# Performance work log

Hardware: AMD Instinct MI355X
Metric: run time of the kernel (lower is better)

Reference implementation:

```python
import jax, jax.numpy as jnp
import numpy as np

NUM_FILTER = 256
CAPS_LEN = 8
NUM_EMOTIONS = 8
OUT_DIM = 16
NUM_CHANNEL = 25
TIME_LEN = 25
NUM_CAPS = NUM_CHANNEL * TIME_LEN * (NUM_FILTER // CAPS_LEN)  # 20000
NUM_ITERATIONS = 3


def setup_inputs() -> dict:
    key = jax.random.key(0)
    ks = jax.random.split(key, 10)
    B = 32
    x = jax.random.normal(ks[0], (B, 54, 54), jnp.float32)
    conv1_w = jax.random.normal(ks[1], (NUM_FILTER, 1, 6, 6), jnp.float32) * 0.05
    conv1_b = jax.random.normal(ks[2], (NUM_FILTER,), jnp.float32) * 0.01
    conv2_w = jax.random.normal(ks[3], (NUM_FILTER, NUM_FILTER, 6, 6), jnp.float32) * 0.01
    conv2_b = jax.random.normal(ks[4], (NUM_FILTER,), jnp.float32) * 0.01
    conv3_w = jax.random.normal(ks[5], (NUM_FILTER, 2 * NUM_FILTER, 1, 1), jnp.float32) * 0.05
    conv3_b = jax.random.normal(ks[6], (NUM_FILTER,), jnp.float32) * 0.01
    # PrimaryCaps: one Linear(caps_len -> caps_len) per capsule, batched as [nc, out, in]
    pc_w = jax.random.normal(ks[7], (NUM_CAPS, CAPS_LEN, CAPS_LEN), jnp.float32) * 0.1
    pc_b = jax.random.normal(ks[8], (NUM_CAPS, CAPS_LEN), jnp.float32) * 0.1
    # EmotionCaps transform W: [nc, num_emotions, out_dim, in_dim]
    W = jax.random.normal(ks[9], (NUM_CAPS, NUM_EMOTIONS, OUT_DIM, CAPS_LEN), jnp.float32) * 0.05
    return {"x": x, "conv1_w": conv1_w, "conv1_b": conv1_b, "conv2_w": conv2_w,
            "conv2_b": conv2_b, "conv3_w": conv3_w, "conv3_b": conv3_b,
            "pc_w": pc_w, "pc_b": pc_b, "W": W}


def _conv(x, w, b, stride):
    y = jax.lax.conv_general_dilated(x, w, (stride, stride), 'VALID',
                                     dimension_numbers=('NCHW', 'OIHW', 'NCHW'))
    return y + b[None, :, None, None]


def _squash(s):
    # scale = |s|^2 / (1 + |s|^2); out = scale * s / (|s| + 1e-8)
    n2 = jnp.sum(s * s, axis=-1, keepdims=True)
    n = jnp.sqrt(n2)
    return (n2 / (1.0 + n2)) * s / (n + 1e-8)


def reference(x, conv1_w, conv1_b, conv2_w, conv2_b, conv3_w, conv3_b, pc_w, pc_b, W):
    x4 = x[:, None]                                    # [B,1,54,54]
    x1 = jax.nn.relu(_conv(x4, conv1_w, conv1_b, 2))   # [B,F,25,25]
    y = jnp.pad(x1, ((0, 0), (0, 0), (2, 3), (2, 3)))  # ZeroPad2d((2,3,2,3))
    y = jax.nn.relu(_conv(y, conv2_w, conv2_b, 1))     # [B,F,25,25]
    z = jax.nn.relu(jnp.concatenate([x1, y], axis=1))  # [B,2F,25,25]
    z = _conv(z, conv3_w, conv3_b, 1)                  # [B,F,25,25]
    B, F, H, Wd = z.shape
    # flatten to capsules: [B, F//caps_len, caps_len, H*W] -> [B, nc, caps_len]
    caps = z.reshape(B, F // CAPS_LEN, CAPS_LEN, H * Wd)
    caps = caps.transpose(0, 1, 3, 2).reshape(B, NUM_CAPS, CAPS_LEN)
    # PrimaryCaps: per-capsule linear, batched as a single einsum
    u = jnp.einsum('bni,noi->bno', caps, pc_w) + pc_b[None]   # [B,nc,caps_len]
    # EmotionCaps: u_hat[b,n,e,o] = W[n,e,o,i] u[b,n,i]
    u_hat = jnp.einsum('bni,neoi->bneo', u, W)                # [B,nc,ne,out_dim]
    b = jnp.zeros((B, NUM_CAPS, NUM_EMOTIONS), u.dtype)
    v = None
    for r in range(NUM_ITERATIONS):
        c = jax.nn.softmax(b, axis=2)[..., None]              # [B,nc,ne,1]
        v = _squash(jnp.sum(c * u_hat, axis=1))               # [B,ne,out_dim]
        if r < NUM_ITERATIONS - 1:
            b = b + jnp.einsum('bneo,beo->bne', u_hat, v)
    return jnp.linalg.norm(v, axis=-1)                        # [B,ne]
```

## Files before the change

kernel.cpp:

```cpp
#include <hip/hip_runtime.h>

typedef unsigned short u16;
typedef __attribute__((ext_vector_type(8))) short bf16x8;
typedef __attribute__((ext_vector_type(4))) float floatx4;

#define NPIX 625
#define NCAPS 20000
#define K2 9216

__device__ __forceinline__ u16 f2bf(float f) {
  unsigned u = __float_as_uint(f);
  return (u16)((u + 0x7fffu + ((u >> 16) & 1u)) >> 16);
}

#define GLDS16(g, l) __builtin_amdgcn_global_load_lds( \
    (const __attribute__((address_space(1))) void*)(g), \
    (__attribute__((address_space(3))) void*)(l), 16, 0, 0)

__global__ void prep_weights(const float* __restrict__ w2, const float* __restrict__ w3,
                             u16* __restrict__ A2, u16* __restrict__ A3) {
  int idx = blockIdx.x * 256 + threadIdx.x;
  if (idx < 256 * 36 * 256) {
    int oc = idx / 9216, r = idx % 9216;
    int t = r >> 8, c = r & 255;
    A2[idx] = f2bf(w2[(oc * 256 + c) * 36 + t]);
  } else {
    int j = idx - 256 * 36 * 256;
    if (j < 256 * 512) A3[j] = f2bf(w3[j]);
  }
}

__global__ void prep_wbs(const float* __restrict__ W, u16* __restrict__ Wbs) {
  int r = blockIdx.x * 256 + threadIdx.x;
  int n = r >> 7, eo = r & 127;
  int e = eo >> 4, o = eo & 15;
  const float* src = W + n * 1024 + eo * 8;
  const float4 v0 = *(const float4*)src;
  const float4 v1 = *(const float4*)(src + 4);
  u16* dst = Wbs + n * 1088 + e * 136 + o * 8;
  ushort4 p0, p1;
  p0.x = f2bf(v0.x); p0.y = f2bf(v0.y); p0.z = f2bf(v0.z); p0.w = f2bf(v0.w);
  p1.x = f2bf(v1.x); p1.y = f2bf(v1.y); p1.z = f2bf(v1.z); p1.w = f2bf(v1.w);
  *(ushort4*)dst = p0;
  *(ushort4*)(dst + 4) = p1;
}

__global__ void conv1_kernel(const float* __restrict__ x, const float* __restrict__ w1,
                             const float* __restrict__ b1, u16* __restrict__ x1p) {
  int blk = blockIdx.x;
  int b = blk / 25, i = blk % 25;
  int f = threadIdx.x;
  float wreg[36];
#pragma unroll
  for (int k = 0; k < 36; k++) wreg[k] = w1[f * 36 + k];
  float bias = b1[f];
  const float* xb = x + b * 54 * 54 + (2 * i) * 54;
  for (int j = 0; j < 25; j++) {
    float acc = bias;
#pragma unroll
    for (int ki = 0; ki < 6; ki++)
#pragma unroll
      for (int kj = 0; kj < 6; kj++)
        acc = fmaf(xb[ki * 54 + 2 * j + kj], wreg[ki * 6 + kj], acc);
    x1p[(((b * 30 + i + 2) * 30) + (j + 2)) * 256 + f] = f2bf(fmaxf(acc, 0.f));
  }
}

__global__ __launch_bounds__(256) void conv2_gemm(const u16* __restrict__ A2,
    const u16* __restrict__ x1p, float* __restrict__ P) {
  __shared__ u16 As0[128 * 32];
  __shared__ u16 Bs0[128 * 32];
  __shared__ u16 As1[128 * 32];
  __shared__ u16 Bs1[128 * 32];
  const int tid = threadIdx.x;
  const int lane = tid & 63, wave = tid >> 6;
  const int mtile = blockIdx.x, ntile = blockIdx.y, kt = blockIdx.z;

  const int seg0 = tid, seg1 = tid + 256;
  const u16* gA0 = A2 + (mtile * 128 + (seg0 >> 2)) * K2 + (seg0 & 3) * 8 + kt * 4608;
  const u16* gA1 = A2 + (mtile * 128 + (seg1 >> 2)) * K2 + (seg1 & 3) * 8 + kt * 4608;

  auto pixbase = [&](int seg) {
    int n = ntile * 128 + (seg >> 2);
    if (n > NCAPS - 1) n = NCAPS - 1;
    int b = n / NPIX, p = n % NPIX;
    int i = p / 25, j = p % 25;
    return ((b * 30 + i) * 30 + j) * 256 + (seg & 3) * 8;
  };
  const u16* gb0 = x1p + pixbase(seg0);
  const u16* gb1 = x1p + pixbase(seg1);

  floatx4 acc[4][4] = {};
  const int wm = wave & 1, wn = wave >> 1;
  const int lrow = lane & 15, kgrp = lane >> 4;

  int kj = 0;
  int boff = 3 * kt * 30 * 256;
  for (int t = 0; t < 18; t++) {
#pragma unroll 1
    for (int cc = 0; cc < 8; cc += 2) {
      const int b0 = boff + cc * 32;
      GLDS16(gA0, As0 + seg0 * 8);
      GLDS16(gA1, As0 + seg1 * 8);
      GLDS16(gA0 + 32, As1 + seg0 * 8);
      GLDS16(gA1 + 32, As1 + seg1 * 8);
      GLDS16(gb0 + b0, Bs0 + seg0 * 8);
      GLDS16(gb1 + b0, Bs0 + seg1 * 8);
      GLDS16(gb0 + b0 + 32, Bs1 + seg0 * 8);
      GLDS16(gb1 + b0 + 32, Bs1 + seg1 * 8);
      gA0 += 64; gA1 += 64;
      __syncthreads();
      bf16x8 af[4], bfr[4];
#pragma unroll
      for (int tt = 0; tt < 4; tt++) {
        af[tt]  = *(const bf16x8*)(As0 + (wm * 64 + tt * 16 + lrow) * 32 + kgrp * 8);
        bfr[tt] = *(const bf16x8*)(Bs0 + (wn * 64 + tt * 16 + lrow) * 32 + kgrp * 8);
      }
#pragma unroll
      for (int tm = 0; tm < 4; tm++)
#pragma unroll
        for (int tn = 0; tn < 4; tn++)
          acc[tm][tn] = __builtin_amdgcn_mfma_f32_16x16x32_bf16(af[tm], bfr[tn], acc[tm][tn], 0, 0, 0);
#pragma unroll
      for (int tt = 0; tt < 4; tt++) {
        af[tt]  = *(const bf16x8*)(As1 + (wm * 64 + tt * 16 + lrow) * 32 + kgrp * 8);
        bfr[tt] = *(const bf16x8*)(Bs1 + (wn * 64 + tt * 16 + lrow) * 32 + kgrp * 8);
      }
#pragma unroll
      for (int tm = 0; tm < 4; tm++)
#pragma unroll
        for (int tn = 0; tn < 4; tn++)
          acc[tm][tn] = __builtin_amdgcn_mfma_f32_16x16x32_bf16(af[tm], bfr[tn], acc[tm][tn], 0, 0, 0);
      __syncthreads();
    }
    boff += 256;
    kj++;
    if (kj == 6) { kj = 0; boff += 6144; }
  }

  float* Pk = P + kt * 5120000;
  const int nb = ntile * 128 + wn * 64;
  const int ocb = mtile * 128 + wm * 64 + kgrp * 4;
#pragma unroll
  for (int tn = 0; tn < 4; tn++) {
    int n = nb + tn * 16 + lrow;
    if (n < NCAPS) {
#pragma unroll
      for (int tm = 0; tm < 4; tm++) {
        int oc = ocb + tm * 16;
        float4 v;
        v.x = acc[tm][tn][0]; v.y = acc[tm][tn][1];
        v.z = acc[tm][tn][2]; v.w = acc[tm][tn][3];
        *(float4*)(Pk + n * 256 + oc) = v;
      }
    }
  }
}

__global__ void conv2_red(const float* __restrict__ P, const float* __restrict__ bias2,
                          u16* __restrict__ y) {
  const int idx = blockIdx.x * 256 + threadIdx.x;
  const float4 a = *(const float4*)(P + idx * 4);
  const float4 b = *(const float4*)(P + 5120000 + idx * 4);
  const float4 bs = *(const float4*)(bias2 + ((idx * 4) & 255));
  ushort4 pk;
  pk.x = f2bf(fmaxf(a.x + b.x + bs.x, 0.f));
  pk.y = f2bf(fmaxf(a.y + b.y + bs.y, 0.f));
  pk.z = f2bf(fmaxf(a.z + b.z + bs.z, 0.f));
  pk.w = f2bf(fmaxf(a.w + b.w + bs.w, 0.f));
  *(ushort4*)(y + idx * 4) = pk;
}

__global__ __launch_bounds__(256) void conv3_gemm(const u16* __restrict__ A3,
    const u16* __restrict__ x1p, const u16* __restrict__ y,
    const float* __restrict__ bias3, float* __restrict__ z) {
  __shared__ u16 As[128 * 32];
  __shared__ u16 Bs[128 * 32];
  const int tid = threadIdx.x;
  const int lane = tid & 63, wave = tid >> 6;
  const int mtile = blockIdx.x, ntile = blockIdx.y;

  const int seg0 = tid, seg1 = tid + 256;
  const u16* ga0 = A3 + (mtile * 128 + (seg0 >> 2)) * 512 + (seg0 & 3) * 8;
  const u16* ga1 = A3 + (mtile * 128 + (seg1 >> 2)) * 512 + (seg1 & 3) * 8;

  auto mkbases = [&](int seg, const u16*& gx, const u16*& gy) {
    int n = ntile * 128 + (seg >> 2);
    if (n > NCAPS - 1) n = NCAPS - 1;
    int b = n / NPIX, p = n % NPIX;
    int i = p / 25, j = p % 25;
    gx = x1p + ((b * 30 + i + 2) * 30 + (j + 2)) * 256 + (seg & 3) * 8;
    gy = y + n * 256 + (seg & 3) * 8;
  };
  const u16 *gx0, *gy0, *gx1, *gy1;
  mkbases(seg0, gx0, gy0);
  mkbases(seg1, gx1, gy1);

  floatx4 acc[4][4] = {};
  const int wm = wave & 1, wn = wave >> 1;
  const int lrow = lane & 15, kgrp = lane >> 4;

  for (int kc = 0; kc < 16; kc++) {
    const u16* s0 = (kc < 8) ? (gx0 + kc * 32) : (gy0 + (kc - 8) * 32);
    const u16* s1 = (kc < 8) ? (gx1 + kc * 32) : (gy1 + (kc - 8) * 32);
    GLDS16(ga0 + kc * 32, As + seg0 * 8);
    GLDS16(ga1 + kc * 32, As + seg1 * 8);
    GLDS16(s0, Bs + seg0 * 8);
    GLDS16(s1, Bs + seg1 * 8);
    __syncthreads();
    bf16x8 af[4], bfr[4];
#pragma unroll
    for (int tt = 0; tt < 4; tt++) {
      af[tt]  = *(const bf16x8*)(As + (wm * 64 + tt * 16 + lrow) * 32 + kgrp * 8);
      bfr[tt] = *(const bf16x8*)(Bs + (wn * 64 + tt * 16 + lrow) * 32 + kgrp * 8);
    }
#pragma unroll
    for (int tm = 0; tm < 4; tm++)
#pragma unroll
      for (int tn = 0; tn < 4; tn++)
        acc[tm][tn] = __builtin_amdgcn_mfma_f32_16x16x32_bf16(af[tm], bfr[tn], acc[tm][tn], 0, 0, 0);
    __syncthreads();
  }

  const int nb = ntile * 128 + wn * 64;
  const int fb = mtile * 128 + wm * 64 + kgrp * 4;
#pragma unroll
  for (int tn = 0; tn < 4; tn++) {
    int n = nb + tn * 16 + lrow;
    if (n < NCAPS) {
#pragma unroll
      for (int tm = 0; tm < 4; tm++) {
        int f0 = fb + tm * 16;
        float4 v;
        v.x = acc[tm][tn][0] + bias3[f0 + 0];
        v.y = acc[tm][tn][1] + bias3[f0 + 1];
        v.z = acc[tm][tn][2] + bias3[f0 + 2];
        v.w = acc[tm][tn][3] + bias3[f0 + 3];
        *(float4*)(z + n * 256 + f0) = v;
      }
    }
  }
}


__device__ __forceinline__ float dot8v(float4 a0, float4 a1, float4 b0, float4 b1) {
  float s = a0.x * b0.x;
  s = fmaf(a0.y, b0.y, s); s = fmaf(a0.z, b0.z, s); s = fmaf(a0.w, b0.w, s);
  s = fmaf(a1.x, b1.x, s); s = fmaf(a1.y, b1.y, s);
  s = fmaf(a1.z, b1.z, s); s = fmaf(a1.w, b1.w, s);
  return s;
}

__device__ __forceinline__ float dotrow(uint4 w, float4 ua, float4 ub) {
  float s = __uint_as_float(w.x << 16) * ua.x;
  s = fmaf(__uint_as_float(w.x & 0xffff0000u), ua.y, s);
  s = fmaf(__uint_as_float(w.y << 16), ua.z, s);
  s = fmaf(__uint_as_float(w.y & 0xffff0000u), ua.w, s);
  s = fmaf(__uint_as_float(w.z << 16), ub.x, s);
  s = fmaf(__uint_as_float(w.z & 0xffff0000u), ub.y, s);
  s = fmaf(__uint_as_float(w.w << 16), ub.z, s);
  s = fmaf(__uint_as_float(w.w & 0xffff0000u), ub.w, s);
  return s;
}

__global__ void caps_u(const float* __restrict__ z, const float* __restrict__ pcw,
                       const float* __restrict__ pcb, float* __restrict__ u) {
  const int tid = threadIdx.x;
  const int b = tid >> 3, o = tid & 7;
  for (int k = 0; k < 8; k++) {
    const int n = blockIdx.x * 8 + k;
    const int g = n / NPIX, p = n % NPIX;
    const float* zp = z + (b * NPIX + p) * 256 + g * 8;
    float4 c0 = *(const float4*)zp;
    float4 c1 = *(const float4*)(zp + 4);
    const float* pw = pcw + n * 64 + o * 8;
    float4 w0 = *(const float4*)pw;
    float4 w1 = *(const float4*)(pw + 4);
    u[n * 256 + tid] = pcb[n * 8 + o] + dot8v(w0, w1, c0, c1);
  }
}

__global__ void caps_u2(const float* __restrict__ z, const float* __restrict__ pcw,
                        const float* __restrict__ pcb, unsigned* __restrict__ u2) {
  const int tid = threadIdx.x;
  const int b = tid >> 3, o = tid & 7;
  for (int k = 0; k < 8; k++) {
    const int n = blockIdx.x * 8 + k;
    const int g = n / NPIX, p = n % NPIX;
    const float* zp = z + (b * NPIX + p) * 256 + g * 8;
    float4 c0 = *(const float4*)zp;
    float4 c1 = *(const float4*)(zp + 4);
    const float* pw = pcw + n * 64 + o * 8;
    float4 w0 = *(const float4*)pw;
    float4 w1 = *(const float4*)(pw + 4);
    const float myu = pcb[n * 8 + o] + dot8v(w0, w1, c0, c1);
    const float partner = __shfl_xor(myu, 1, 64);
    if (!(o & 1)) {
      unsigned pk = (unsigned)f2bf(myu) | ((unsigned)f2bf(partner) << 16);
      u2[n * 128 + b * 4 + (o >> 1)] = pk;
    }
  }
}

__global__ __launch_bounds__(256, 4) void caps_accb2(const unsigned* __restrict__ u2,
    const u16* __restrict__ Wbs, const float* __restrict__ vsum,
    float* __restrict__ Spart) {
  __shared__ u16 Ws[16 * 1088];
  const int tid = threadIdx.x;
  const int b = tid >> 3, e = tid & 7;
  const int n0 = blockIdx.x * 16;

  const u16* gsrc = Wbs + n0 * 1088;
#pragma unroll
  for (int k = 0; k < 9; k++) {
    const int idx = k * 256 + tid;
    if (idx < 2176) GLDS16(gsrc + idx * 8, Ws + idx * 8);
  }

  const float* vp = vsum + tid * 16;
  const float4 V0 = *(const float4*)vp;
  const float4 V1 = *(const float4*)(vp + 4);
  const float4 V2 = *(const float4*)(vp + 8);
  const float4 V3 = *(const float4*)(vp + 12);
  float s0 = 0.f, s1 = 0.f, s2 = 0.f, s3 = 0.f, s4 = 0.f, s5 = 0.f, s6 = 0.f, s7 = 0.f;
  float s8 = 0.f, s9 = 0.f, s10 = 0.f, s11 = 0.f, s12 = 0.f, s13 = 0.f, s14 = 0.f, s15 = 0.f;

  __syncthreads();

  for (int it = 0; it < 16; it++) {
    const int n = n0 + it;
    const uint4 up = *(const uint4*)(u2 + n * 128 + b * 4);
    float4 ua, ub;
    ua.x = __uint_as_float(up.x << 16); ua.y = __uint_as_float(up.x & 0xffff0000u);
    ua.z = __uint_as_float(up.y << 16); ua.w = __uint_as_float(up.y & 0xffff0000u);
    ub.x = __uint_as_float(up.z << 16); ub.y = __uint_as_float(up.z & 0xffff0000u);
    ub.z = __uint_as_float(up.w << 16); ub.w = __uint_as_float(up.w & 0xffff0000u);

    const u16* Wn = Ws + it * 1088 + e * 136;
    float h0, h1, h2, h3, h4, h5, h6, h7, h8, h9, h10, h11, h12, h13, h14, h15;
#define ROW(o, H) { uint4 w = *(const uint4*)(Wn + (o) * 8); H = dotrow(w, ua, ub); }
    ROW(0, h0)   ROW(1, h1)   ROW(2, h2)   ROW(3, h3)
    ROW(4, h4)   ROW(5, h5)   ROW(6, h6)   ROW(7, h7)
    ROW(8, h8)   ROW(9, h9)   ROW(10, h10) ROW(11, h11)
    ROW(12, h12) ROW(13, h13) ROW(14, h14) ROW(15, h15)
#undef ROW
    float blog = h0 * V0.x;
    blog = fmaf(h1, V0.y, blog);  blog = fmaf(h2, V0.z, blog);  blog = fmaf(h3, V0.w, blog);
    blog = fmaf(h4, V1.x, blog);  blog = fmaf(h5, V1.y, blog);  blog = fmaf(h6, V1.z, blog);
    blog = fmaf(h7, V1.w, blog);  blog = fmaf(h8, V2.x, blog);  blog = fmaf(h9, V2.y, blog);
    blog = fmaf(h10, V2.z, blog); blog = fmaf(h11, V2.w, blog); blog = fmaf(h12, V3.x, blog);
    blog = fmaf(h13, V3.y, blog); blog = fmaf(h14, V3.z, blog); blog = fmaf(h15, V3.w, blog);
    float m = blog;
    m = fmaxf(m, __shfl_xor(m, 1, 64));
    m = fmaxf(m, __shfl_xor(m, 2, 64));
    m = fmaxf(m, __shfl_xor(m, 4, 64));
    float ex = __expf(blog - m);
    float ss = ex;
    ss += __shfl_xor(ss, 1, 64);
    ss += __shfl_xor(ss, 2, 64);
    ss += __shfl_xor(ss, 4, 64);
    const float c = ex / ss;
    s0 = fmaf(c, h0, s0);   s1 = fmaf(c, h1, s1);   s2 = fmaf(c, h2, s2);   s3 = fmaf(c, h3, s3);
    s4 = fmaf(c, h4, s4);   s5 = fmaf(c, h5, s5);   s6 = fmaf(c, h6, s6);   s7 = fmaf(c, h7, s7);
    s8 = fmaf(c, h8, s8);   s9 = fmaf(c, h9, s9);   s10 = fmaf(c, h10, s10); s11 = fmaf(c, h11, s11);
    s12 = fmaf(c, h12, s12); s13 = fmaf(c, h13, s13); s14 = fmaf(c, h14, s14); s15 = fmaf(c, h15, s15);
  }
  float* Sp = Spart + blockIdx.x * 4096 + tid * 16;
  *(float4*)(Sp + 0)  = make_float4(s0, s1, s2, s3);
  *(float4*)(Sp + 4)  = make_float4(s4, s5, s6, s7);
  *(float4*)(Sp + 8)  = make_float4(s8, s9, s10, s11);
  *(float4*)(Sp + 12) = make_float4(s12, s13, s14, s15);
}

__global__ __launch_bounds__(256, 2) void caps_acc(const float* __restrict__ u,
    const float* __restrict__ W, const float* __restrict__ vsum,
    float* __restrict__ Spart) {
  const int tid = threadIdx.x;
  const int b = tid >> 3, e = tid & 7;
  const float* vp = vsum + tid * 16;
  const float4 V0 = *(const float4*)vp;
  const float4 V1 = *(const float4*)(vp + 4);
  const float4 V2 = *(const float4*)(vp + 8);
  const float4 V3 = *(const float4*)(vp + 12);
  float s0 = 0.f, s1 = 0.f, s2 = 0.f, s3 = 0.f, s4 = 0.f, s5 = 0.f, s6 = 0.f, s7 = 0.f;
  float s8 = 0.f, s9 = 0.f, s10 = 0.f, s11 = 0.f, s12 = 0.f, s13 = 0.f, s14 = 0.f, s15 = 0.f;
  const int n0 = blockIdx.x * 16;
  for (int it = 0; it < 16; it++) {
    const int n = n0 + it;
    const float* un = u + n * 256 + (b << 3);
    const float4 u0 = *(const float4*)un;
    const float4 u1 = *(const float4*)(un + 4);
    const float* Wn = W + n * 1024 + e * 128;
    float h0, h1, h2, h3, h4, h5, h6, h7, h8, h9, h10, h11, h12, h13, h14, h15;
#define OST(o, H) { float4 wa = *(const float4*)(Wn + (o) * 8); \
                    float4 wb = *(const float4*)(Wn + (o) * 8 + 4); \
                    H = dot8v(wa, wb, u0, u1); }
    OST(0, h0)  OST(1, h1)  OST(2, h2)  OST(3, h3)
    OST(4, h4)  OST(5, h5)  OST(6, h6)  OST(7, h7)
    OST(8, h8)  OST(9, h9)  OST(10, h10) OST(11, h11)
    OST(12, h12) OST(13, h13) OST(14, h14) OST(15, h15)
#undef OST
    float blog = h0 * V0.x;
    blog = fmaf(h1, V0.y, blog);  blog = fmaf(h2, V0.z, blog);  blog = fmaf(h3, V0.w, blog);
    blog = fmaf(h4, V1.x, blog);  blog = fmaf(h5, V1.y, blog);  blog = fmaf(h6, V1.z, blog);
    blog = fmaf(h7, V1.w, blog);  blog = fmaf(h8, V2.x, blog);  blog = fmaf(h9, V2.y, blog);
    blog = fmaf(h10, V2.z, blog); blog = fmaf(h11, V2.w, blog); blog = fmaf(h12, V3.x, blog);
    blog = fmaf(h13, V3.y, blog); blog = fmaf(h14, V3.z, blog); blog = fmaf(h15, V3.w, blog);
    float m = blog;
    m = fmaxf(m, __shfl_xor(m, 1, 64));
    m = fmaxf(m, __shfl_xor(m, 2, 64));
    m = fmaxf(m, __shfl_xor(m, 4, 64));
    float ex = __expf(blog - m);
    float ss = ex;
    ss += __shfl_xor(ss, 1, 64);
    ss += __shfl_xor(ss, 2, 64);
    ss += __shfl_xor(ss, 4, 64);
    const float c = ex / ss;
    s0 = fmaf(c, h0, s0);   s1 = fmaf(c, h1, s1);   s2 = fmaf(c, h2, s2);   s3 = fmaf(c, h3, s3);
    s4 = fmaf(c, h4, s4);   s5 = fmaf(c, h5, s5);   s6 = fmaf(c, h6, s6);   s7 = fmaf(c, h7, s7);
    s8 = fmaf(c, h8, s8);   s9 = fmaf(c, h9, s9);   s10 = fmaf(c, h10, s10); s11 = fmaf(c, h11, s11);
    s12 = fmaf(c, h12, s12); s13 = fmaf(c, h13, s13); s14 = fmaf(c, h14, s14); s15 = fmaf(c, h15, s15);
  }
  float* Sp = Spart + blockIdx.x * 4096 + tid * 16;
  *(float4*)(Sp + 0)  = make_float4(s0, s1, s2, s3);
  *(float4*)(Sp + 4)  = make_float4(s4, s5, s6, s7);
  *(float4*)(Sp + 8)  = make_float4(s8, s9, s10, s11);
  *(float4*)(Sp + 12) = make_float4(s12, s13, s14, s15);
}

__global__ void caps_redA(const float* __restrict__ Spart, float* __restrict__ S) {
  const int j = blockIdx.x * 256 + threadIdx.x;
  const int r0 = blockIdx.y * 50;
  float a0 = 0.f, a1 = 0.f;
  for (int r = 0; r < 50; r += 2) {
    a0 += Spart[(r0 + r) * 4096 + j];
    a1 += Spart[(r0 + r + 1) * 4096 + j];
  }
  atomicAdd(&S[j], a0 + a1);
}

__global__ void caps_v(const float* __restrict__ S, float* __restrict__ vsum, int add) {
  const int t = threadIdx.x;
  const float* sp = S + t * 16;
  const float4 a0 = *(const float4*)sp;
  const float4 a1 = *(const float4*)(sp + 4);
  const float4 a2 = *(const float4*)(sp + 8);
  const float4 a3 = *(const float4*)(sp + 12);
  float n2 = a0.x * a0.x;
  n2 = fmaf(a0.y, a0.y, n2); n2 = fmaf(a0.z, a0.z, n2); n2 = fmaf(a0.w, a0.w, n2);
  n2 = fmaf(a1.x, a1.x, n2); n2 = fmaf(a1.y, a1.y, n2); n2 = fmaf(a1.z, a1.z, n2); n2 = fmaf(a1.w, a1.w, n2);
  n2 = fmaf(a2.x, a2.x, n2); n2 = fmaf(a2.y, a2.y, n2); n2 = fmaf(a2.z, a2.z, n2); n2 = fmaf(a2.w, a2.w, n2);
  n2 = fmaf(a3.x, a3.x, n2); n2 = fmaf(a3.y, a3.y, n2); n2 = fmaf(a3.z, a3.z, n2); n2 = fmaf(a3.w, a3.w, n2);
  const float n = sqrtf(n2);
  const float scale = n2 / ((1.f + n2) * (n + 1e-8f));
  float* vp = vsum + t * 16;
  float4 o0, o1, o2, o3;
  if (add) {
    o0 = *(float4*)(vp + 0); o1 = *(float4*)(vp + 4); o2 = *(float4*)(vp + 8); o3 = *(float4*)(vp + 12);
  } else {
    o0 = make_float4(0.f, 0.f, 0.f, 0.f); o1 = o0; o2 = o0; o3 = o0;
  }
  o0.x = fmaf(a0.x, scale, o0.x); o0.y = fmaf(a0.y, scale, o0.y);
  o0.z = fmaf(a0.z, scale, o0.z); o0.w = fmaf(a0.w, scale, o0.w);
  o1.x = fmaf(a1.x, scale, o1.x); o1.y = fmaf(a1.y, scale, o1.y);
  o1.z = fmaf(a1.z, scale, o1.z); o1.w = fmaf(a1.w, scale, o1.w);
  o2.x = fmaf(a2.x, scale, o2.x); o2.y = fmaf(a2.y, scale, o2.y);
  o2.z = fmaf(a2.z, scale, o2.z); o2.w = fmaf(a2.w, scale, o2.w);
  o3.x = fmaf(a3.x, scale, o3.x); o3.y = fmaf(a3.y, scale, o3.y);
  o3.z = fmaf(a3.z, scale, o3.z); o3.w = fmaf(a3.w, scale, o3.w);
  *(float4*)(vp + 0) = o0; *(float4*)(vp + 4) = o1;
  *(float4*)(vp + 8) = o2; *(float4*)(vp + 12) = o3;
}

__global__ void caps_out(const float* __restrict__ S, float* __restrict__ out) {
  const int t = threadIdx.x;
  const float* sp = S + t * 16;
  const float4 a0 = *(const float4*)sp;
  const float4 a1 = *(const float4*)(sp + 4);
  const float4 a2 = *(const float4*)(sp + 8);
  const float4 a3 = *(const float4*)(sp + 12);
  float n2 = a0.x * a0.x;
  n2 = fmaf(a0.y, a0.y, n2); n2 = fmaf(a0.z, a0.z, n2); n2 = fmaf(a0.w, a0.w, n2);
  n2 = fmaf(a1.x, a1.x, n2); n2 = fmaf(a1.y, a1.y, n2); n2 = fmaf(a1.z, a1.z, n2); n2 = fmaf(a1.w, a1.w, n2);
  n2 = fmaf(a2.x, a2.x, n2); n2 = fmaf(a2.y, a2.y, n2); n2 = fmaf(a2.z, a2.z, n2); n2 = fmaf(a2.w, a2.w, n2);
  n2 = fmaf(a3.x, a3.x, n2); n2 = fmaf(a3.y, a3.y, n2); n2 = fmaf(a3.z, a3.z, n2); n2 = fmaf(a3.w, a3.w, n2);
  const float n = sqrtf(n2);
  out[t] = n * n2 / ((1.f + n2) * (n + 1e-8f));
}

extern "C" void kernel_launch(void* const* d_in, const int* in_sizes, int n_in,
                              void* d_out, int out_size, void* d_ws, size_t ws_size,
                              hipStream_t stream) {
  const float* x   = (const float*)d_in[0];
  const float* w1  = (const float*)d_in[1];
  const float* b1  = (const float*)d_in[2];
  const float* w2  = (const float*)d_in[3];
  const float* b2  = (const float*)d_in[4];
  const float* w3  = (const float*)d_in[5];
  const float* b3  = (const float*)d_in[6];
  const float* pcw = (const float*)d_in[7];
  const float* pcb = (const float*)d_in[8];
  const float* W   = (const float*)d_in[9];
  float* out = (float*)d_out;

  char* ws = (char*)d_ws;
  const bool use_bf16w = (ws_size >= (size_t)75000000);

  u16*   x1p = (u16*)(ws + 0);
  u16*   A2  = (u16*)(ws + 14745600);
  u16*   A3  = (u16*)(ws + 19464192);
  u16*   y   = (u16*)(ws + 19726336);
  float* P   = (float*)(ws + 29966336);

  u16* Wbs;
  unsigned* u2;
  float *z, *Spart, *u, *S, *vs;
  if (use_bf16w) {
    Wbs   = (u16*)(ws + 0);
    z     = (float*)(ws + 43520000);
    Spart = (float*)(ws + 43520000);
    u2    = (unsigned*)(ws + 64000000);
    S     = (float*)(ws + 74240000);
    vs    = (float*)(ws + 74256384);
    u = nullptr;
  } else {
    Wbs = nullptr; u2 = nullptr;
    z     = (float*)(ws + 29966336);
    Spart = (float*)(ws + 29966336);
    u     = (float*)(ws + 50446336);
    S     = (float*)(ws + 70926336);
    vs    = (float*)(ws + 70942720);
  }

  hipMemsetAsync(x1p, 0, 14745600, stream);
  hipMemsetAsync(vs, 0, 16384, stream);

  prep_weights<<<9728, 256, 0, stream>>>(w2, w3, A2, A3);
  conv1_kernel<<<800, 256, 0, stream>>>(x, w1, b1, x1p);
  conv2_gemm<<<dim3(2, 157, 2), 256, 0, stream>>>(A2, x1p, P);
  conv2_red<<<5000, 256, 0, stream>>>(P, b2, y);
  conv3_gemm<<<dim3(2, 157), 256, 0, stream>>>(A3, x1p, y, b3, z);
  if (use_bf16w) {
    prep_wbs<<<10000, 256, 0, stream>>>(W, Wbs);
    caps_u2<<<2500, 256, 0, stream>>>(z, pcw, pcb, u2);
  } else {
    caps_u<<<2500, 256, 0, stream>>>(z, pcw, pcb, u);
  }

  for (int pass = 0; pass < 3; pass++) {
    if (use_bf16w)
      caps_accb2<<<1250, 256, 0, stream>>>(u2, Wbs, vs, Spart);
    else
      caps_acc<<<1250, 256, 0, stream>>>(u, W, vs, Spart);
    hipMemsetAsync(S, 0, 16384, stream);
    caps_redA<<<dim3(16, 25), 256, 0, stream>>>(Spart, S);
    if (pass == 0)      caps_v<<<1, 256, 0, stream>>>(S, vs, 0);
    else if (pass == 1) caps_v<<<1, 256, 0, stream>>>(S, vs, 1);
    else                caps_out<<<1, 256, 0, stream>>>(S, out);
  }
}
```

Baseline: 523.3 us.

## Split conv2 GEMM K four ways with XCD-aware mapping, bf16 partials, vectorized weight prep

```diff
diff --git a/kernel.cpp b/kernel.cpp
--- a/kernel.cpp
+++ b/kernel.cpp
@@ -13,20 +13,34 @@
   return (u16)((u + 0x7fffu + ((u >> 16) & 1u)) >> 16);
 }
 
+__device__ __forceinline__ float bf2f(unsigned v) {
+  return __uint_as_float(v << 16);
+}
+
 #define GLDS16(g, l) __builtin_amdgcn_global_load_lds( \
     (const __attribute__((address_space(1))) void*)(g), \
     (__attribute__((address_space(3))) void*)(l), 16, 0, 0)
 
-__global__ void prep_weights(const float* __restrict__ w2, const float* __restrict__ w3,
-                             u16* __restrict__ A2, u16* __restrict__ A3) {
-  int idx = blockIdx.x * 256 + threadIdx.x;
-  if (idx < 256 * 36 * 256) {
-    int oc = idx / 9216, r = idx % 9216;
-    int t = r >> 8, c = r & 255;
-    A2[idx] = f2bf(w2[(oc * 256 + c) * 36 + t]);
+__global__ void prep_weights2(const float* __restrict__ w2, const float* __restrict__ w3,
+                              u16* __restrict__ A2, u16* __restrict__ A3) {
+  if (blockIdx.x < 256) {
+    const int oc = blockIdx.x, c = threadIdx.x;
+    const float* src = w2 + (oc * 256 + c) * 36;
+    float v[36];
+#pragma unroll
+    for (int k = 0; k < 9; k++) {
+      const float4 q = *(const float4*)(src + k * 4);
+      v[k * 4 + 0] = q.x; v[k * 4 + 1] = q.y; v[k * 4 + 2] = q.z; v[k * 4 + 3] = q.w;
+    }
+    u16* dst = A2 + oc * 9216 + c;
+#pragma unroll
+    for (int t = 0; t < 36; t++) dst[t * 256] = f2bf(v[t]);
   } else {
-    int j = idx - 256 * 36 * 256;
-    if (j < 256 * 512) A3[j] = f2bf(w3[j]);
+    const int j = (blockIdx.x - 256) * 1024 + threadIdx.x * 4;
+    const float4 q = *(const float4*)(w3 + j);
+    ushort4 p;
+    p.x = f2bf(q.x); p.y = f2bf(q.y); p.z = f2bf(q.z); p.w = f2bf(q.w);
+    *(ushort4*)(A3 + j) = p;
   }
 }
 
@@ -67,18 +81,21 @@
 }
 
 __global__ __launch_bounds__(256) void conv2_gemm(const u16* __restrict__ A2,
-    const u16* __restrict__ x1p, float* __restrict__ P) {
+    const u16* __restrict__ x1p, u16* __restrict__ P) {
   __shared__ u16 As0[128 * 32];
   __shared__ u16 Bs0[128 * 32];
   __shared__ u16 As1[128 * 32];
   __shared__ u16 Bs1[128 * 32];
   const int tid = threadIdx.x;
   const int lane = tid & 63, wave = tid >> 6;
-  const int mtile = blockIdx.x, ntile = blockIdx.y, kt = blockIdx.z;
+  const int f = blockIdx.x;
+  const int xcd = f & 7, ntile = f >> 3;
+  const int kt = xcd >> 1, mtile = xcd & 1;
+  const int t0 = kt * 9;
 
   const int seg0 = tid, seg1 = tid + 256;
-  const u16* gA0 = A2 + (mtile * 128 + (seg0 >> 2)) * K2 + (seg0 & 3) * 8 + kt * 4608;
-  const u16* gA1 = A2 + (mtile * 128 + (seg1 >> 2)) * K2 + (seg1 & 3) * 8 + kt * 4608;
+  const u16* gA0 = A2 + (mtile * 128 + (seg0 >> 2)) * K2 + (seg0 & 3) * 8 + t0 * 256;
+  const u16* gA1 = A2 + (mtile * 128 + (seg1 >> 2)) * K2 + (seg1 & 3) * 8 + t0 * 256;
 
   auto pixbase = [&](int seg) {
     int n = ntile * 128 + (seg >> 2);
@@ -94,9 +111,9 @@
   const int wm = wave & 1, wn = wave >> 1;
   const int lrow = lane & 15, kgrp = lane >> 4;
 
-  int kj = 0;
-  int boff = 3 * kt * 30 * 256;
-  for (int t = 0; t < 18; t++) {
+  int kj = t0 % 6;
+  int boff = ((t0 / 6) * 30 + kj) * 256;
+  for (int t = 0; t < 9; t++) {
 #pragma unroll 1
     for (int cc = 0; cc < 8; cc += 2) {
       const int b0 = boff + cc * 32;
@@ -138,7 +155,7 @@
     if (kj == 6) { kj = 0; boff += 6144; }
   }
 
-  float* Pk = P + kt * 5120000;
+  u16* Pk = P + kt * 5120000;
   const int nb = ntile * 128 + wn * 64;
   const int ocb = mtile * 128 + wm * 64 + kgrp * 4;
 #pragma unroll
@@ -148,26 +165,34 @@
 #pragma unroll
       for (int tm = 0; tm < 4; tm++) {
         int oc = ocb + tm * 16;
-        float4 v;
-        v.x = acc[tm][tn][0]; v.y = acc[tm][tn][1];
-        v.z = acc[tm][tn][2]; v.w = acc[tm][tn][3];
-        *(float4*)(Pk + n * 256 + oc) = v;
+        ushort4 pk;
+        pk.x = f2bf(acc[tm][tn][0]);
+        pk.y = f2bf(acc[tm][tn][1]);
+        pk.z = f2bf(acc[tm][tn][2]);
+        pk.w = f2bf(acc[tm][tn][3]);
+        *(ushort4*)(Pk + n * 256 + oc) = pk;
       }
     }
   }
 }
 
-__global__ void conv2_red(const float* __restrict__ P, const float* __restrict__ bias2,
+__global__ void conv2_red(const u16* __restrict__ P, const float* __restrict__ bias2,
                           u16* __restrict__ y) {
   const int idx = blockIdx.x * 256 + threadIdx.x;
-  const float4 a = *(const float4*)(P + idx * 4);
-  const float4 b = *(const float4*)(P + 5120000 + idx * 4);
+  const ushort4 p0 = *(const ushort4*)(P + idx * 4);
+  const ushort4 p1 = *(const ushort4*)(P + 5120000 + idx * 4);
+  const ushort4 p2 = *(const ushort4*)(P + 10240000 + idx * 4);
+  const ushort4 p3 = *(const ushort4*)(P + 15360000 + idx * 4);
   const float4 bs = *(const float4*)(bias2 + ((idx * 4) & 255));
+  float sx = bf2f(p0.x) + bf2f(p1.x) + bf2f(p2.x) + bf2f(p3.x) + bs.x;
+  float sy = bf2f(p0.y) + bf2f(p1.y) + bf2f(p2.y) + bf2f(p3.y) + bs.y;
+  float sz = bf2f(p0.z) + bf2f(p1.z) + bf2f(p2.z) + bf2f(p3.z) + bs.z;
+  float sw = bf2f(p0.w) + bf2f(p1.w) + bf2f(p2.w) + bf2f(p3.w) + bs.w;
   ushort4 pk;
-  pk.x = f2bf(fmaxf(a.x + b.x + bs.x, 0.f));
-  pk.y = f2bf(fmaxf(a.y + b.y + bs.y, 0.f));
-  pk.z = f2bf(fmaxf(a.z + b.z + bs.z, 0.f));
-  pk.w = f2bf(fmaxf(a.w + b.w + bs.w, 0.f));
+  pk.x = f2bf(fmaxf(sx, 0.f));
+  pk.y = f2bf(fmaxf(sy, 0.f));
+  pk.z = f2bf(fmaxf(sz, 0.f));
+  pk.w = f2bf(fmaxf(sw, 0.f));
   *(ushort4*)(y + idx * 4) = pk;
 }
 
@@ -510,7 +535,7 @@
   u16*   A2  = (u16*)(ws + 14745600);
   u16*   A3  = (u16*)(ws + 19464192);
   u16*   y   = (u16*)(ws + 19726336);
-  float* P   = (float*)(ws + 29966336);
+  u16*   P   = (u16*)(ws + 29966336);
 
   u16* Wbs;
   unsigned* u2;
@@ -535,9 +560,9 @@
   hipMemsetAsync(x1p, 0, 14745600, stream);
   hipMemsetAsync(vs, 0, 16384, stream);
 
-  prep_weights<<<9728, 256, 0, stream>>>(w2, w3, A2, A3);
+  prep_weights2<<<384, 256, 0, stream>>>(w2, w3, A2, A3);
   conv1_kernel<<<800, 256, 0, stream>>>(x, w1, b1, x1p);
-  conv2_gemm<<<dim3(2, 157, 2), 256, 0, stream>>>(A2, x1p, P);
+  conv2_gemm<<<1256, 256, 0, stream>>>(A2, x1p, P);
   conv2_red<<<5000, 256, 0, stream>>>(P, b2, y);
   conv3_gemm<<<dim3(2, 157), 256, 0, stream>>>(A3, x1p, y, b3, z);
   if (use_bf16w) {
```

Measured after the change: 510.9 us. 2.4% less time.
